# Performance work log

Hardware: AMD Instinct MI355X
Metric: run time of the kernel (lower is better)

## Reference

```python
import jax, jax.numpy as jnp
import numpy as np

T, B, I, H, LBL = 200, 1024, 128, 128, 4


def setup_inputs() -> dict:
    key = jax.random.key(0)
    ks = jax.random.split(key, 14)
    si = 1.0 / np.sqrt(I)
    sh = 1.0 / np.sqrt(H)
    inputs = jax.random.normal(ks[0], (T, B, I), jnp.float32)
    lengths = jnp.maximum(jax.random.randint(ks[1], (B,), 1, T + 1), LBL).astype(jnp.int32)
    return {
        "inputs": inputs,
        "lengths": lengths,
        "Wih_g": jax.random.normal(ks[2], (3 * H, I), jnp.float32) * si,
        "Whh_g": jax.random.normal(ks[3], (3 * H, H), jnp.float32) * sh,
        "bih_g": jax.random.normal(ks[4], (3 * H,), jnp.float32) * sh,
        "bhh_g": jax.random.normal(ks[5], (3 * H,), jnp.float32) * sh,
        "Wih_l": jax.random.normal(ks[6], (3 * H, I), jnp.float32) * si,
        "Whh_l": jax.random.normal(ks[7], (3 * H, H), jnp.float32) * sh,
        "bih_l": jax.random.normal(ks[8], (3 * H,), jnp.float32) * sh,
        "bhh_l": jax.random.normal(ks[9], (3 * H,), jnp.float32) * sh,
        "A1": jax.random.normal(ks[10], (H, H), jnp.float32) * sh,
        "A2": jax.random.normal(ks[11], (H, H), jnp.float32) * sh,
        "v1": jax.random.normal(ks[12], (1, H), jnp.float32) * sh,
        "label_len": LBL,
    }


def gru(x, Wih, Whh, bih, bhh):
    # x: [T, B, I] time-major. PyTorch GRU cell semantics.
    Bq, Hq = x.shape[1], Whh.shape[1]
    gi_all = jnp.einsum('tbi,gi->tbg', x, Wih) + bih  # precompute input projections [T,B,3H]
    def step(h, gi):
        gh = h @ Whh.T + bhh
        ir, iz, inn = jnp.split(gi, 3, axis=-1)
        hr, hz, hn = jnp.split(gh, 3, axis=-1)
        r = jax.nn.sigmoid(ir + hr)
        z = jax.nn.sigmoid(iz + hz)
        n = jnp.tanh(inn + r * hn)
        h = (1.0 - z) * n + z * h
        return h, h
    h0 = jnp.zeros((Bq, Hq), x.dtype)
    _, hs = jax.lax.scan(step, h0, gi_all)
    return hs  # [T, B, H]


def reference(inputs, lengths, Wih_g, Whh_g, bih_g, bhh_g,
              Wih_l, Whh_l, bih_l, bhh_l, A1, A2, v1, label_len):
    h_g = gru(inputs, Wih_g, Whh_g, bih_g, bhh_g)  # [T,B,H]
    h_l = gru(inputs, Wih_l, Whh_l, bih_l, bhh_l)  # [T,B,H]
    # attention score per step s: v1(sigmoid(A1 h_l + A2 h_g)), query-independent
    pre = jax.nn.sigmoid(jnp.einsum('tbh,gh->tbg', h_l, A1) +
                         jnp.einsum('tbh,gh->tbg', h_g, A2))
    scores = jnp.einsum('tbg,og->tbo', pre, v1)  # [T,B,1]
    # per-t output = cumsum_{s<=t}(score*h_l) + h_g[t]
    out = jnp.cumsum(scores * h_l, axis=0) + h_g  # [T,B,H]
    out_b = jnp.transpose(out, (1, 0, 2))  # [B,T,H]
    # gather last label_len timesteps of each sequence: h[b,k] = out[L_b-label_len+k, b]
    idx = lengths[:, None].astype(jnp.int32) - label_len + jnp.arange(label_len, dtype=jnp.int32)[None, :]
    idx = jnp.clip(idx, 0, out_b.shape[1] - 1)  # [B, label_len]
    h = jnp.take_along_axis(out_b, idx[:, :, None], axis=1)  # [B, label_len, H]
    return h
```

## Files before the change

kernel.cpp:

```cpp
#include <hip/hip_runtime.h>
#include <stdint.h>


typedef __attribute__((ext_vector_type(8))) short short8;
typedef __attribute__((ext_vector_type(4))) float float4v;

#define LDS_BARRIER() asm volatile("s_waitcnt lgkmcnt(0)\n\ts_barrier" ::: "memory")

__device__ inline float bf2f(unsigned short u){
  union { unsigned int i; float f; } v; v.i = ((unsigned int)u) << 16; return v.f;
}
__device__ inline unsigned short f2bf(float f){
  union { float f; unsigned int i; } v; v.f = f;
  unsigned int x = v.i;
  return (unsigned short)((x + 0x7fffu + ((x >> 16) & 1u)) >> 16);
}
__device__ inline unsigned int pack2(float a, float b){
  return (unsigned int)f2bf(a) | ((unsigned int)f2bf(b) << 16);
}
__device__ inline float sigm(float x){ return __builtin_amdgcn_rcpf(1.0f + __expf(-x)); }

__global__ void k_prep(unsigned short* hl_slot, unsigned short* hg_slot, float* cum,
                       const float* A1, const float* A2, unsigned short* a12)
{
  int i = blockIdx.x * blockDim.x + threadIdx.x;
  hl_slot[i] = 0;
  hg_slot[i] = 0;
  cum[i] = 0.0f;
  if (i < 32768) {
    a12[i] = f2bf((i < 16384) ? A1[i] : A2[i - 16384]);
  }
}

__global__ void k_xcast(const float* __restrict__ x, unsigned short* __restrict__ xb)
{
  size_t i = (size_t)blockIdx.x * blockDim.x + threadIdx.x;
  const float4* xf = (const float4*)x;
  float4 a = xf[2 * i], b = xf[2 * i + 1];
  short8 o;
  o[0]=(short)f2bf(a.x); o[1]=(short)f2bf(a.y); o[2]=(short)f2bf(a.z); o[3]=(short)f2bf(a.w);
  o[4]=(short)f2bf(b.x); o[5]=(short)f2bf(b.y); o[6]=(short)f2bf(b.z); o[7]=(short)f2bf(b.w);
  *(short8*)(xb + i * 8) = o;
}

__global__ __launch_bounds__(512, 2) void k_scan(
    const unsigned short* __restrict__ xb,
    const float* __restrict__ Wih_g, const float* __restrict__ Whh_g,
    const float* __restrict__ bih_g, const float* __restrict__ bhh_g,
    const float* __restrict__ Wih_l, const float* __restrict__ Whh_l,
    const float* __restrict__ bih_l, const float* __restrict__ bhh_l,
    unsigned short* __restrict__ hl_seq, unsigned short* __restrict__ hg_seq,
    int tc, int t0)
{
  __shared__ __align__(16) unsigned short hb[2][2048];
  int tid = threadIdx.x;
  int w = tid >> 6, L = tid & 63, l15 = L & 15, q = L >> 4;
  int gru = blockIdx.x & 1;
  int b0 = (blockIdx.x >> 1) * 16;
  const float* Wih = gru ? Wih_l : Wih_g;
  const float* Whh = gru ? Whh_l : Whh_g;
  const float* bih = gru ? bih_l : bih_g;
  const float* bhh = gru ? bhh_l : bhh_g;
  unsigned short* myseq = gru ? hl_seq : hg_seq;

  int col = w * 16 + l15;

  short8 Wi[3][4], Wh[3][4];
  #pragma unroll
  for (int G = 0; G < 3; G++) {
    int row = G * 128 + col;
    #pragma unroll
    for (int kf = 0; kf < 4; kf++) {
      const float4* p0 = (const float4*)(Wih + (size_t)row * 128 + kf * 32 + q * 8);
      const float4* p1 = (const float4*)(Whh + (size_t)row * 128 + kf * 32 + q * 8);
      float4 a0 = p0[0], a1 = p0[1], b0f = p1[0], b1f = p1[1];
      short8 si, sh;
      si[0]=(short)f2bf(a0.x); si[1]=(short)f2bf(a0.y); si[2]=(short)f2bf(a0.z); si[3]=(short)f2bf(a0.w);
      si[4]=(short)f2bf(a1.x); si[5]=(short)f2bf(a1.y); si[6]=(short)f2bf(a1.z); si[7]=(short)f2bf(a1.w);
      sh[0]=(short)f2bf(b0f.x); sh[1]=(short)f2bf(b0f.y); sh[2]=(short)f2bf(b0f.z); sh[3]=(short)f2bf(b0f.w);
      sh[4]=(short)f2bf(b1f.x); sh[5]=(short)f2bf(b1f.y); sh[6]=(short)f2bf(b1f.z); sh[7]=(short)f2bf(b1f.w);
      Wi[G][kf] = si; Wh[G][kf] = sh;
    }
  }
  float br  = bih[col]       + bhh[col];
  float bz  = bih[128 + col] + bhh[128 + col];
  float bin = bih[256 + col];
  float bnh = bhh[256 + col];

  float hold[4];
  #pragma unroll
  for (int r = 0; r < 4; r++) {
    int m = q * 4 + r;
    unsigned short u = myseq[((size_t)(tc - 1) * 1024 + b0 + m) * 128 + col];
    hold[r] = bf2f(u);
    hb[0][(col >> 3) * 128 + m * 8 + (col & 7)] = u;
  }

  short8 x2[2][4];
  const unsigned short* xlane = xb + ((size_t)b0 + l15) * 128 + q * 8;
  {
    const unsigned short* px = xlane + (size_t)t0 * 131072;
    #pragma unroll
    for (int kf = 0; kf < 4; kf++) x2[0][kf] = *(const short8*)(px + kf * 32);
    int t1 = t0 + (tc > 1 ? 1 : 0);
    const unsigned short* py = xlane + (size_t)t1 * 131072;
    #pragma unroll
    for (int kf = 0; kf < 4; kf++) x2[1][kf] = *(const short8*)(py + kf * 32);
  }
  __syncthreads();

  unsigned short* opq = myseq + ((size_t)(b0 + q * 4)) * 128 + col;
  unsigned int* hbw = (unsigned int*)&hb[0][0];
  int wdw = (2 * w + (l15 >> 3)) * 64 + ((l15 & 6) >> 1);
  bool wlane = (L & 1) == 0;

  auto step = [&](int s, int pin, int pout) {
    short8 Ah[4];
    #pragma unroll
    for (int kf = 0; kf < 4; kf++)
      Ah[kf] = *(const short8*)&hb[pin][(kf * 4 + q) * 128 + l15 * 8];

    float4v rx = (float4v){0.f,0.f,0.f,0.f}, zx = rx, nx = rx;
    #pragma unroll
    for (int kf = 0; kf < 4; kf++) rx = __builtin_amdgcn_mfma_f32_16x16x32_bf16(x2[pin][kf], Wi[0][kf], rx, 0,0,0);
    #pragma unroll
    for (int kf = 0; kf < 4; kf++) zx = __builtin_amdgcn_mfma_f32_16x16x32_bf16(x2[pin][kf], Wi[1][kf], zx, 0,0,0);
    #pragma unroll
    for (int kf = 0; kf < 4; kf++) nx = __builtin_amdgcn_mfma_f32_16x16x32_bf16(x2[pin][kf], Wi[2][kf], nx, 0,0,0);

    {
      int t2 = t0 + (s + 2 < tc ? s + 2 : tc - 1);
      const unsigned short* px = xlane + (size_t)t2 * 131072;
      #pragma unroll
      for (int kf = 0; kf < 4; kf++) x2[pin][kf] = *(const short8*)(px + kf * 32);
    }

    float4v rh = (float4v){0.f,0.f,0.f,0.f}, zh = rh, nh = rh;
    #pragma unroll
    for (int kf = 0; kf < 4; kf++) rh = __builtin_amdgcn_mfma_f32_16x16x32_bf16(Ah[kf], Wh[0][kf], rh, 0,0,0);
    #pragma unroll
    for (int kf = 0; kf < 4; kf++) zh = __builtin_amdgcn_mfma_f32_16x16x32_bf16(Ah[kf], Wh[1][kf], zh, 0,0,0);
    #pragma unroll
    for (int kf = 0; kf < 4; kf++) nh = __builtin_amdgcn_mfma_f32_16x16x32_bf16(Ah[kf], Wh[2][kf], nh, 0,0,0);

    float cr[4], cz[4], cn[4];
    #pragma unroll
    for (int r = 0; r < 4; r++) { cr[r] = rx[r] + br; cz[r] = zx[r] + bz; cn[r] = nx[r] + bin; }

    unsigned int* hbo = hbw + pout * 1024 + wdw;
    #pragma unroll
    for (int r = 0; r < 4; r++) {
      float er = __expf(-(rh[r] + cr[r]));
      float ez = __expf(-(zh[r] + cz[r]));
      float pr = 1.0f + er, pz = 1.0f + ez;
      float inv = __builtin_amdgcn_rcpf(pr * pz);
      float rr = pz * inv;
      float zz = pr * inv;
      float y  = cn[r] + rr * (nh[r] + bnh);
      float em = __expf(-2.0f * y);
      float nn = 2.0f * __builtin_amdgcn_rcpf(1.0f + em) - 1.0f;
      float hn = nn + zz * (hold[r] - nn);
      hold[r] = hn;
      unsigned short hu = f2bf(hn);
      opq[r * 128] = hu;
      unsigned int hv = (unsigned int)hu;
      unsigned int ov = (unsigned int)__shfl_xor((int)hv, 1);
      if (wlane) hbo[(4 * q + r) * 4] = hv | (ov << 16);
    }
    opq += 131072;
    LDS_BARRIER();
  };

  int s = 0;
  for (; s + 1 < tc; s += 2) { step(s, 0, 1); step(s + 1, 1, 0); }
  if (s < tc) step(s, 0, 1);
}

__global__ __launch_bounds__(512) void k_score(const unsigned short* __restrict__ hl_seq,
                                               const unsigned short* __restrict__ hg_seq,
                                               const unsigned short* __restrict__ a12,
                                               const float* __restrict__ v1,
                                               float* __restrict__ score, int tc)
{
  __shared__ __align__(16) unsigned short M1[128][136];
  __shared__ __align__(16) unsigned short M2[128][136];
  int tid = threadIdx.x;
  int w = tid >> 6, L = tid & 63;
  int l15 = L & 15, q = L >> 4;
  int s = blockIdx.x;
  int bhalf = blockIdx.y * 512;

  #pragma unroll
  for (int it = 0; it < 4; it++) {
    int f8 = it * 512 + tid;
    *(short8*)&M1[f8 >> 4][(f8 & 15) * 8] = *(const short8*)(a12 + (size_t)f8 * 8);
    *(short8*)&M2[f8 >> 4][(f8 & 15) * 8] = *(const short8*)(a12 + 16384 + (size_t)f8 * 8);
  }
  __syncthreads();

  float v1v[8];
  #pragma unroll
  for (int nt = 0; nt < 8; nt++) v1v[nt] = v1[nt * 16 + l15];

  short8 Fl[4], Fg[4], Pl[4], Pg[4];
  {
    size_t base = ((size_t)s * 1024 + bhalf + (size_t)w * 16 + l15) * 128;
    #pragma unroll
    for (int kf = 0; kf < 4; kf++) {
      Fl[kf] = *(const short8*)(hl_seq + base + kf * 32 + q * 8);
      Fg[kf] = *(const short8*)(hg_seq + base + kf * 32 + q * 8);
    }
  }
  #pragma unroll
  for (int it = 0; it < 4; it++) {
    int b0 = bhalf + (it * 8 + w) * 16;
    if (it + 1 < 4) {
      size_t base = ((size_t)s * 1024 + bhalf + (size_t)((it + 1) * 8 + w) * 16 + l15) * 128;
      #pragma unroll
      for (int kf = 0; kf < 4; kf++) {
        Pl[kf] = *(const short8*)(hl_seq + base + kf * 32 + q * 8);
        Pg[kf] = *(const short8*)(hg_seq + base + kf * 32 + q * 8);
      }
    }
    float4v acc[8];
    #pragma unroll
    for (int nt = 0; nt < 8; nt++) {
      float4v a = (float4v){0.f, 0.f, 0.f, 0.f};
      #pragma unroll
      for (int kf = 0; kf < 4; kf++)
        a = __builtin_amdgcn_mfma_f32_16x16x32_bf16(
            Fl[kf], *(const short8*)&M1[nt * 16 + l15][kf * 32 + q * 8], a, 0, 0, 0);
      #pragma unroll
      for (int kf = 0; kf < 4; kf++)
        a = __builtin_amdgcn_mfma_f32_16x16x32_bf16(
            Fg[kf], *(const short8*)&M2[nt * 16 + l15][kf * 32 + q * 8], a, 0, 0, 0);
      acc[nt] = a;
    }
    float p4[4];
    #pragma unroll
    for (int r = 0; r < 4; r++) {
      float sum = 0.f;
      #pragma unroll
      for (int nt = 0; nt < 8; nt++) sum += v1v[nt] * sigm(acc[nt][r]);
      sum += __shfl_xor(sum, 1, 16);
      sum += __shfl_xor(sum, 2, 16);
      sum += __shfl_xor(sum, 4, 16);
      sum += __shfl_xor(sum, 8, 16);
      p4[r] = sum;
    }
    if (l15 == 0) {
      #pragma unroll
      for (int r = 0; r < 4; r++)
        score[(size_t)(b0 + q * 4 + r) * tc + s] = p4[r];
    }
    #pragma unroll
    for (int kf = 0; kf < 4; kf++) { Fl[kf] = Pl[kf]; Fg[kf] = Pg[kf]; }
  }
}

__global__ __launch_bounds__(256) void k_cum(const float* __restrict__ score,
                                             const unsigned short* __restrict__ hl_seq,
                                             const unsigned short* __restrict__ hg_seq,
                                             const int* __restrict__ lengths,
                                             float* __restrict__ cum,
                                             float* __restrict__ out, int tc, int t0)
{
  __shared__ __align__(16) unsigned short hlL[100 * 256];
  __shared__ float scL[2][100];
  int tid = threadIdx.x;
  int b2 = tid >> 7, j = tid & 127;
  int b0 = blockIdx.x * 2;
  int b = b0 + b2;
  int base = b2 * 128 + j;

  float c = cum[(size_t)b * 128 + j];
  int cap0 = lengths[b] - 4;

  float hgv[4];
  #pragma unroll
  for (int d = 0; d < 4; d++) {
    int sl = cap0 + d - t0;
    hgv[d] = (sl >= 0 && sl < tc) ? bf2f(hg_seq[((size_t)sl * 1024 + b) * 128 + j]) : 0.f;
  }

  for (int seg = 0; seg < tc; seg += 100) {
    int len = (tc - seg < 100) ? (tc - seg) : 100;
    __syncthreads();
    for (int f8 = tid; f8 < len * 32; f8 += 256) {
      int sl = f8 >> 5, r8 = f8 & 31;
      *(short8*)&hlL[(size_t)f8 * 8] =
          *(const short8*)(hl_seq + ((size_t)(seg + sl) * 1024 + b0) * 128 + r8 * 8);
    }
    for (int i = tid; i < 2 * len; i += 256) {
      int bb = (i >= len) ? 1 : 0;
      int sl = i - bb * len;
      scL[bb][sl] = score[(size_t)(b0 + bb) * tc + seg + sl];
    }
    __syncthreads();

    int sl = 0;
    for (; sl + 5 <= len; sl += 5) {
      float h[5], sc[5];
      #pragma unroll
      for (int k = 0; k < 5; k++) {
        h[k] = bf2f(hlL[(size_t)(sl + k) * 256 + base]);
        sc[k] = scL[b2][sl + k];
      }
      #pragma unroll
      for (int k = 0; k < 5; k++) {
        c += sc[k] * h[k];
        int d = (t0 + seg + sl + k) - cap0;
        if ((unsigned)d < 4u)
          out[((size_t)b * 4 + d) * 128 + j] = c + hgv[d];
      }
    }
    for (; sl < len; sl++) {
      c += scL[b2][sl] * bf2f(hlL[(size_t)sl * 256 + base]);
      int d = (t0 + seg + sl) - cap0;
      if ((unsigned)d < 4u)
        out[((size_t)b * 4 + d) * 128 + j] = c + hgv[d];
    }
  }
  cum[(size_t)b * 128 + j] = c;
}

extern "C" void kernel_launch(void* const* d_in, const int* in_sizes, int n_in,
                              void* d_out, int out_size, void* d_ws, size_t ws_size,
                              hipStream_t stream)
{
  const float* x     = (const float*)d_in[0];
  const int* lengths = (const int*)d_in[1];
  const float* Wih_g = (const float*)d_in[2];
  const float* Whh_g = (const float*)d_in[3];
  const float* bih_g = (const float*)d_in[4];
  const float* bhh_g = (const float*)d_in[5];
  const float* Wih_l = (const float*)d_in[6];
  const float* Whh_l = (const float*)d_in[7];
  const float* bih_l = (const float*)d_in[8];
  const float* bhh_l = (const float*)d_in[9];
  const float* A1    = (const float*)d_in[10];
  const float* A2    = (const float*)d_in[11];
  const float* v1    = (const float*)d_in[12];
  float* out = (float*)d_out;

  const size_t XB = (size_t)200 * 1024 * 128 * 2;
  const size_t fixed = 65536 + 524288 + XB;
  const int cands[8] = {200, 100, 50, 25, 10, 5, 2, 1};
  int tc = 0;
  for (int i = 0; i < 8; i++) {
    int T = cands[i];
    size_t need = 2 * (size_t)T * 1024 * 128 * 2
                + (size_t)T * 1024 * 4
                + fixed;
    if (need <= ws_size) { tc = T; break; }
  }
  if (!tc) return;

  char* wsb = (char*)d_ws;
  size_t o = 0;
  unsigned short* a12 = (unsigned short*)(wsb + o); o += 65536;
  float* cum   = (float*)(wsb + o); o += 524288;
  unsigned short* xb = (unsigned short*)(wsb + o); o += XB;
  unsigned short* hl  = (unsigned short*)(wsb + o); o += (size_t)tc * 1024 * 128 * 2;
  unsigned short* hg  = (unsigned short*)(wsb + o); o += (size_t)tc * 1024 * 128 * 2;
  float* score = (float*)(wsb + o);

  unsigned short* hl_slot = hl + (size_t)(tc - 1) * 1024 * 128;
  unsigned short* hg_slot = hg + (size_t)(tc - 1) * 1024 * 128;

  k_prep<<<512, 256, 0, stream>>>(hl_slot, hg_slot, cum, A1, A2, a12);
  k_xcast<<<12800, 256, 0, stream>>>(x, xb);
  int nch = 200 / tc;
  for (int c = 0; c < nch; c++) {
    k_scan<<<128, 512, 0, stream>>>(xb, Wih_g, Whh_g, bih_g, bhh_g,
                                    Wih_l, Whh_l, bih_l, bhh_l, hl, hg, tc, c * tc);
    k_score<<<dim3(tc, 2), 512, 0, stream>>>(hl, hg, a12, v1, score, tc);
    k_cum<<<512, 256, 0, stream>>>(score, hl, hg, lengths, cum, out, tc, c * tc);
  }
}
```

Before: 432.0 us.

## Tile x and hidden-state buffers into 16-row chunked layout for coalesced fragment loads

Changes the global layout of the bf16 input copy and the hl/hg sequence buffers from row-major [t][b][h] to a tiled [t][bgroup][chunk8][m16][8] layout. The xcast kernel writes this tiled layout, and the scan, score and cum kernels index into it. MFMA operand fragments (16 rows x 8 elements per quarter-wave) become contiguous 256-byte runs, and the scan's per-step hidden-state stores become more contiguous. The cum kernel's per-sequence reads become more scattered in exchange, and the xcast store pattern changes.

```diff
diff --git a/kernel.cpp b/kernel.cpp
--- a/kernel.cpp
+++ b/kernel.cpp
@@ -14,9 +14,6 @@
   union { float f; unsigned int i; } v; v.f = f;
   unsigned int x = v.i;
   return (unsigned short)((x + 0x7fffu + ((x >> 16) & 1u)) >> 16);
-}
-__device__ inline unsigned int pack2(float a, float b){
-  return (unsigned int)f2bf(a) | ((unsigned int)f2bf(b) << 16);
 }
 __device__ inline float sigm(float x){ return __builtin_amdgcn_rcpf(1.0f + __expf(-x)); }
 
@@ -34,13 +31,17 @@
 
 __global__ void k_xcast(const float* __restrict__ x, unsigned short* __restrict__ xb)
 {
-  size_t i = (size_t)blockIdx.x * blockDim.x + threadIdx.x;
-  const float4* xf = (const float4*)x;
-  float4 a = xf[2 * i], b = xf[2 * i + 1];
+  int i8 = blockIdx.x * blockDim.x + threadIdx.x;
+  int t = i8 >> 14;
+  int rem = i8 & 16383;
+  int b = rem >> 4, c = rem & 15;
+  int m = b & 15, bg = b >> 4;
+  const float4* xf = (const float4*)(x + ((size_t)t * 131072 + (size_t)b * 128 + c * 8));
+  float4 a = xf[0], bb = xf[1];
   short8 o;
   o[0]=(short)f2bf(a.x); o[1]=(short)f2bf(a.y); o[2]=(short)f2bf(a.z); o[3]=(short)f2bf(a.w);
-  o[4]=(short)f2bf(b.x); o[5]=(short)f2bf(b.y); o[6]=(short)f2bf(b.z); o[7]=(short)f2bf(b.w);
-  *(short8*)(xb + i * 8) = o;
+  o[4]=(short)f2bf(bb.x); o[5]=(short)f2bf(bb.y); o[6]=(short)f2bf(bb.z); o[7]=(short)f2bf(bb.w);
+  *(short8*)(xb + (size_t)t * 131072 + (size_t)bg * 2048 + c * 128 + m * 8) = o;
 }
 
 __global__ __launch_bounds__(512, 2) void k_scan(
@@ -56,7 +57,7 @@
   int tid = threadIdx.x;
   int w = tid >> 6, L = tid & 63, l15 = L & 15, q = L >> 4;
   int gru = blockIdx.x & 1;
-  int b0 = (blockIdx.x >> 1) * 16;
+  int bg = blockIdx.x >> 1;
   const float* Wih = gru ? Wih_l : Wih_g;
   const float* Whh = gru ? Whh_l : Whh_g;
   const float* bih = gru ? bih_l : bih_g;
@@ -64,6 +65,8 @@
   unsigned short* myseq = gru ? hl_seq : hg_seq;
 
   int col = w * 16 + l15;
+  int cch = w * 2 + (l15 >> 3);
+  int cj  = l15 & 7;
 
   short8 Wi[3][4], Wh[3][4];
   #pragma unroll
@@ -91,25 +94,25 @@
   #pragma unroll
   for (int r = 0; r < 4; r++) {
     int m = q * 4 + r;
-    unsigned short u = myseq[((size_t)(tc - 1) * 1024 + b0 + m) * 128 + col];
+    unsigned short u = myseq[(size_t)(tc - 1) * 131072 + (size_t)bg * 2048 + cch * 128 + m * 8 + cj];
     hold[r] = bf2f(u);
-    hb[0][(col >> 3) * 128 + m * 8 + (col & 7)] = u;
+    hb[0][cch * 128 + m * 8 + cj] = u;
   }
 
   short8 x2[2][4];
-  const unsigned short* xlane = xb + ((size_t)b0 + l15) * 128 + q * 8;
+  const unsigned short* xlane = xb + (size_t)bg * 2048 + q * 128 + l15 * 8;
   {
     const unsigned short* px = xlane + (size_t)t0 * 131072;
     #pragma unroll
-    for (int kf = 0; kf < 4; kf++) x2[0][kf] = *(const short8*)(px + kf * 32);
+    for (int kf = 0; kf < 4; kf++) x2[0][kf] = *(const short8*)(px + kf * 512);
     int t1 = t0 + (tc > 1 ? 1 : 0);
     const unsigned short* py = xlane + (size_t)t1 * 131072;
     #pragma unroll
-    for (int kf = 0; kf < 4; kf++) x2[1][kf] = *(const short8*)(py + kf * 32);
+    for (int kf = 0; kf < 4; kf++) x2[1][kf] = *(const short8*)(py + kf * 512);
   }
   __syncthreads();
 
-  unsigned short* opq = myseq + ((size_t)(b0 + q * 4)) * 128 + col;
+  unsigned short* opq = myseq + (size_t)bg * 2048 + cch * 128 + q * 32 + cj;
   unsigned int* hbw = (unsigned int*)&hb[0][0];
   int wdw = (2 * w + (l15 >> 3)) * 64 + ((l15 & 6) >> 1);
   bool wlane = (L & 1) == 0;
@@ -132,7 +135,7 @@
       int t2 = t0 + (s + 2 < tc ? s + 2 : tc - 1);
       const unsigned short* px = xlane + (size_t)t2 * 131072;
       #pragma unroll
-      for (int kf = 0; kf < 4; kf++) x2[pin][kf] = *(const short8*)(px + kf * 32);
+      for (int kf = 0; kf < 4; kf++) x2[pin][kf] = *(const short8*)(px + kf * 512);
     }
 
     float4v rh = (float4v){0.f,0.f,0.f,0.f}, zh = rh, nh = rh;
@@ -162,7 +165,7 @@
       float hn = nn + zz * (hold[r] - nn);
       hold[r] = hn;
       unsigned short hu = f2bf(hn);
-      opq[r * 128] = hu;
+      opq[r * 8] = hu;
       unsigned int hv = (unsigned int)hu;
       unsigned int ov = (unsigned int)__shfl_xor((int)hv, 1);
       if (wlane) hbo[(4 * q + r) * 4] = hv | (ov << 16);
@@ -188,7 +191,7 @@
   int w = tid >> 6, L = tid & 63;
   int l15 = L & 15, q = L >> 4;
   int s = blockIdx.x;
-  int bhalf = blockIdx.y * 512;
+  int bghalf = blockIdx.y * 32;
 
   #pragma unroll
   for (int it = 0; it < 4; it++) {
@@ -204,22 +207,22 @@
 
   short8 Fl[4], Fg[4], Pl[4], Pg[4];
   {
-    size_t base = ((size_t)s * 1024 + bhalf + (size_t)w * 16 + l15) * 128;
+    size_t base = (size_t)s * 131072 + (size_t)(bghalf + w) * 2048 + q * 128 + l15 * 8;
     #pragma unroll
     for (int kf = 0; kf < 4; kf++) {
-      Fl[kf] = *(const short8*)(hl_seq + base + kf * 32 + q * 8);
-      Fg[kf] = *(const short8*)(hg_seq + base + kf * 32 + q * 8);
+      Fl[kf] = *(const short8*)(hl_seq + base + kf * 512);
+      Fg[kf] = *(const short8*)(hg_seq + base + kf * 512);
     }
   }
   #pragma unroll
   for (int it = 0; it < 4; it++) {
-    int b0 = bhalf + (it * 8 + w) * 16;
+    int bg = bghalf + it * 8 + w;
     if (it + 1 < 4) {
-      size_t base = ((size_t)s * 1024 + bhalf + (size_t)((it + 1) * 8 + w) * 16 + l15) * 128;
+      size_t base = (size_t)s * 131072 + (size_t)(bghalf + (it + 1) * 8 + w) * 2048 + q * 128 + l15 * 8;
       #pragma unroll
       for (int kf = 0; kf < 4; kf++) {
-        Pl[kf] = *(const short8*)(hl_seq + base + kf * 32 + q * 8);
-        Pg[kf] = *(const short8*)(hg_seq + base + kf * 32 + q * 8);
+        Pl[kf] = *(const short8*)(hl_seq + base + kf * 512);
+        Pg[kf] = *(const short8*)(hg_seq + base + kf * 512);
       }
     }
     float4v acc[8];
@@ -251,7 +254,7 @@
     if (l15 == 0) {
       #pragma unroll
       for (int r = 0; r < 4; r++)
-        score[(size_t)(b0 + q * 4 + r) * tc + s] = p4[r];
+        score[(size_t)(bg * 16 + q * 4 + r) * tc + s] = p4[r];
     }
     #pragma unroll
     for (int kf = 0; kf < 4; kf++) { Fl[kf] = Pl[kf]; Fg[kf] = Pg[kf]; }
@@ -272,6 +275,7 @@
   int b0 = blockIdx.x * 2;
   int b = b0 + b2;
   int base = b2 * 128 + j;
+  int bg0 = b0 >> 4, m0 = b0 & 15;
 
   float c = cum[(size_t)b * 128 + j];
   int cap0 = lengths[b] - 4;
@@ -280,7 +284,9 @@
   #pragma unroll
   for (int d = 0; d < 4; d++) {
     int sl = cap0 + d - t0;
-    hgv[d] = (sl >= 0 && sl < tc) ? bf2f(hg_seq[((size_t)sl * 1024 + b) * 128 + j]) : 0.f;
+    hgv[d] = (sl >= 0 && sl < tc)
+      ? bf2f(hg_seq[(size_t)sl * 131072 + (size_t)(b >> 4) * 2048 + (j >> 3) * 128 + (b & 15) * 8 + (j & 7)])
+      : 0.f;
   }
 
   for (int seg = 0; seg < tc; seg += 100) {
@@ -288,8 +294,10 @@
     __syncthreads();
     for (int f8 = tid; f8 < len * 32; f8 += 256) {
       int sl = f8 >> 5, r8 = f8 & 31;
+      int bb = r8 >> 4, ch = r8 & 15;
       *(short8*)&hlL[(size_t)f8 * 8] =
-          *(const short8*)(hl_seq + ((size_t)(seg + sl) * 1024 + b0) * 128 + r8 * 8);
+          *(const short8*)(hl_seq + (size_t)(seg + sl) * 131072 + (size_t)bg0 * 2048
+                           + ch * 128 + (m0 + bb) * 8);
     }
     for (int i = tid; i < 2 * len; i += 256) {
       int bb = (i >= len) ? 1 : 0;
```

Result: slower. 444.0 us (+2.8%).
